# Kernel optimization log

Measured on AMD Instinct MI355X. Metric: run time of the kernel, lower is better.

The kernel has to match this reference:

```python
import jax, jax.numpy as jnp
import numpy as np

DIM = 768
HEADS = 12
E = 8
TOPK = 2
EPS = 1e-5


def layer_norm(x, g, b):
    m = jnp.mean(x, axis=-1, keepdims=True)
    v = jnp.mean((x - m) ** 2, axis=-1, keepdims=True)
    return (x - m) * jax.lax.rsqrt(v + EPS) * g + b


def setup_inputs() -> dict:
    key = jax.random.key(0)
    ks = jax.random.split(key, 12)
    B, N, C = 16, 1024, DIM
    s = 0.02
    return {
        "x": jax.random.normal(ks[0], (B, N, C), jnp.float32),
        "noise": jax.random.normal(ks[1], (B, N, E), jnp.float32),
        "ln1_g": jnp.ones((C,), jnp.float32),
        "ln1_b": jnp.zeros((C,), jnp.float32),
        "qkv_w": jax.random.normal(ks[2], (C, 3 * C), jnp.float32) * s,  # pre-transposed
        "proj_w": jax.random.normal(ks[3], (C, C), jnp.float32) * s,
        "proj_b": jnp.zeros((C,), jnp.float32),
        "ln2_g": jnp.ones((C,), jnp.float32),
        "ln2_b": jnp.zeros((C,), jnp.float32),
        "route_w": jax.random.normal(ks[4], (C, E), jnp.float32) * s,
        "route_b": jnp.zeros((E,), jnp.float32),
        "rln_g": jnp.ones((E,), jnp.float32),
        "rln_b": jnp.zeros((E,), jnp.float32),
        "expert_w": jax.random.normal(ks[5], (E, C, C), jnp.float32) * s,  # [E, in, out]
        "expert_b": jnp.zeros((E, C), jnp.float32),
    }


def reference(x, noise, ln1_g, ln1_b, qkv_w, proj_w, proj_b, ln2_g, ln2_b,
              route_w, route_b, rln_g, rln_b, expert_w, expert_b):
    B, N, C = x.shape
    H = HEADS
    Dh = C // H
    scale = Dh ** -0.5

    # --- Attention branch ---
    h = layer_norm(x, ln1_g, ln1_b)
    qkv = (h @ qkv_w).reshape(B, N, 3, H, Dh)
    q, k, v = qkv[:, :, 0], qkv[:, :, 1], qkv[:, :, 2]  # [B,N,H,Dh]
    attn = jnp.einsum('bnhd,bmhd->bhnm', q, k) * scale
    attn = jax.nn.softmax(attn, axis=-1)
    o = jnp.einsum('bhnm,bmhd->bnhd', attn, v).reshape(B, N, C)
    x = x + o @ proj_w + proj_b

    # --- MoE branch ---
    h = layer_norm(x, ln2_g, ln2_b)
    logits = layer_norm(h @ route_w + route_b, rln_g, rln_b)  # [B,N,E]
    rw = jax.nn.softmax(logits, axis=-1) + noise * (1.0 / E)
    topk_w, topk_idx = jax.lax.top_k(rw, TOPK)               # [B,N,K]
    topk_w = jax.nn.softmax(topk_w, axis=-1)

    # dense all-expert compute (faithful to source): [B,N,E,C]
    expert_out = jnp.einsum('bnc,ecd->bned', h, expert_w) + expert_b
    selected = jnp.take_along_axis(expert_out, topk_idx[..., None], axis=2)  # [B,N,K,C]
    moe = jnp.sum(selected * topk_w[..., None], axis=2)
    return x + moe
```

## Files before the change

kernel.cpp:

```cpp
#include <hip/hip_runtime.h>
#include <hip/hip_fp16.h>

typedef unsigned short u16;
typedef unsigned int u32;
typedef _Float16 f16;
typedef short bf16x8 __attribute__((ext_vector_type(8)));
typedef f16 f16x8 __attribute__((ext_vector_type(8)));
typedef float f32x4 __attribute__((ext_vector_type(4)));
typedef u32 u32x4 __attribute__((ext_vector_type(4)));

#define TOKENS 16384
#define CDIM 768
#define NEXP 8

#define QSCALE 0.18033688011112043f

__device__ __forceinline__ u16 f2b(float f) {
  u32 u = __float_as_uint(f);
  return (u16)((u + 0x7fffu + ((u >> 16) & 1u)) >> 16);
}
__device__ __forceinline__ u16 f16bits(f16 x) {
  union { f16 f; u16 u; } c;
  c.f = x;
  return c.u;
}
__device__ __forceinline__ f32x4 mfma_bf(bf16x8 a, bf16x8 b, f32x4 c) {
  return __builtin_amdgcn_mfma_f32_16x16x32_bf16(a, b, c, 0, 0, 0);
}
__device__ __forceinline__ f32x4 mfma_h(f16x8 a, f16x8 b, f32x4 c) {
  return __builtin_amdgcn_mfma_f32_16x16x32_f16(a, b, c, 0, 0, 0);
}
__device__ __forceinline__ void split8(const float* v, f16x8& h, f16x8& l) {
#pragma unroll
  for (int i = 0; i < 8; i++) {
    const f16 hh = (f16)v[i];
    h[i] = hh;
    l[i] = (f16)(v[i] - (float)hh);
  }
}

__global__ __launch_bounds__(256) void transpose_split_f16(
    const float* __restrict__ in, f16* __restrict__ oh, f16* __restrict__ ol,
    int K, int N) {
  __shared__ float tile[64][65];
  const int n0 = blockIdx.x * 64, k0 = blockIdx.y * 64;
#pragma unroll
  for (int i = 0; i < 16; i++) {
    const int s = threadIdx.x + i * 256;
    const int r = s >> 6, c = s & 63;
    tile[r][c] = in[(size_t)(k0 + r) * N + n0 + c];
  }
  __syncthreads();
#pragma unroll
  for (int i = 0; i < 16; i++) {
    const int s = threadIdx.x + i * 256;
    const int r = s >> 6, c = s & 63;
    const float v = tile[c][r];
    const f16 h = (f16)v;
    oh[(size_t)(n0 + r) * K + k0 + c] = h;
    ol[(size_t)(n0 + r) * K + k0 + c] = (f16)(v - (float)h);
  }
}

__global__ __launch_bounds__(256) void transpose_f32_bf16(
    const float* __restrict__ in, u16* __restrict__ out, int K, int N) {
  __shared__ u16 tile[64][65];
  const int z = blockIdx.z;
  in += (size_t)z * K * N;
  out += (size_t)z * K * N;
  const int n0 = blockIdx.x * 64, k0 = blockIdx.y * 64;
#pragma unroll
  for (int i = 0; i < 16; i++) {
    const int s = threadIdx.x + i * 256;
    const int r = s >> 6, c = s & 63;
    tile[r][c] = f2b(in[(size_t)(k0 + r) * N + n0 + c]);
  }
  __syncthreads();
#pragma unroll
  for (int i = 0; i < 16; i++) {
    const int s = threadIdx.x + i * 256;
    const int r = s >> 6, c = s & 63;
    out[(size_t)(n0 + r) * K + k0 + c] = tile[c][r];
  }
}

template <bool BF16OUT>
__global__ __launch_bounds__(256) void ln_rows(const float* __restrict__ in,
                                               const float* __restrict__ g,
                                               const float* __restrict__ bt,
                                               void* __restrict__ out) {
  const int row = blockIdx.x * 4 + (threadIdx.x >> 6);
  const int lane = threadIdx.x & 63;
  const size_t base = (size_t)row * CDIM;
  float v[12];
  float s = 0.f, ss = 0.f;
#pragma unroll
  for (int j = 0; j < 12; j++) {
    const int idx = lane + j * 64;
    v[j] = in[base + idx];
    s += v[j];
    ss += v[j] * v[j];
  }
#pragma unroll
  for (int m = 1; m < 64; m <<= 1) {
    s += __shfl_xor(s, m);
    ss += __shfl_xor(ss, m);
  }
  const float mean = s * (1.f / CDIM);
  const float var = ss * (1.f / CDIM) - mean * mean;
  const float rs = rsqrtf(var + 1e-5f);
#pragma unroll
  for (int j = 0; j < 12; j++) {
    const int idx = lane + j * 64;
    const float y = (v[j] - mean) * rs * g[idx] + bt[idx];
    if (BF16OUT)
      ((u16*)out)[base + idx] = f2b(y);
    else
      ((float*)out)[base + idx] = y;
  }
}

template <int EPI>
__global__ __launch_bounds__(256) void gemm_f16s(
    const float* __restrict__ A, const f16* __restrict__ Bth,
    const f16* __restrict__ Btl, float* __restrict__ C, int M, int N, int K,
    const float* __restrict__ bias, const float* __restrict__ xres,
    f16* __restrict__ Oh, f16* __restrict__ Ol, u32* __restrict__ Ov) {
  __shared__ f16 Ah[128 * 64];
  __shared__ f16 Al[128 * 64];
  __shared__ f16 Bh[128 * 64];
  __shared__ f16 Bl[128 * 64];
  const int tid = threadIdx.x;
  const int lane = tid & 63, wv = tid >> 6;
  const int wr = wv >> 1, wc = wv & 1;
  const int lm = lane & 15, lq = lane >> 4;
  const int m0 = blockIdx.y * 128, n0 = blockIdx.x * 128;
  f32x4 acc[4][4];
  const f32x4 z4 = {0.f, 0.f, 0.f, 0.f};
#pragma unroll
  for (int i = 0; i < 4; i++)
#pragma unroll
    for (int j = 0; j < 4; j++) acc[i][j] = z4;

  for (int k0 = 0; k0 < K; k0 += 64) {
    __syncthreads();
#pragma unroll
    for (int i = 0; i < 4; i++) {
      const int s = tid + i * 256;
      const int r = s >> 3, g = s & 7;
      float av[8];
      *(float4*)&av[0] = *(const float4*)(A + (size_t)(m0 + r) * K + k0 + g * 8);
      *(float4*)&av[4] =
          *(const float4*)(A + (size_t)(m0 + r) * K + k0 + g * 8 + 4);
      f16x8 hh, ll;
      split8(av, hh, ll);
      const int sw = r * 64 + ((g ^ (r & 7)) << 3);
      *(f16x8*)(&Ah[sw]) = hh;
      *(f16x8*)(&Al[sw]) = ll;
      *(f16x8*)(&Bh[sw]) = *(const f16x8*)(Bth + (size_t)(n0 + r) * K + k0 + g * 8);
      *(f16x8*)(&Bl[sw]) = *(const f16x8*)(Btl + (size_t)(n0 + r) * K + k0 + g * 8);
    }
    __syncthreads();
#pragma unroll
    for (int kx = 0; kx < 8; kx += 4) {
      f16x8 afh[4], afl[4], bfh[4], bfl[4];
#pragma unroll
      for (int i = 0; i < 4; i++) {
        const int ra = wr * 64 + i * 16 + lm;
        const int aw = ra * 64 + (((ra & 7) ^ (kx + lq)) << 3);
        afh[i] = *(const f16x8*)(&Ah[aw]);
        afl[i] = *(const f16x8*)(&Al[aw]);
        const int rb = wc * 64 + i * 16 + lm;
        const int bw = rb * 64 + (((rb & 7) ^ (kx + lq)) << 3);
        bfh[i] = *(const f16x8*)(&Bh[bw]);
        bfl[i] = *(const f16x8*)(&Bl[bw]);
      }
#pragma unroll
      for (int i = 0; i < 4; i++)
#pragma unroll
        for (int j = 0; j < 4; j++) {
          acc[i][j] = mfma_h(afh[i], bfh[j], acc[i][j]);
          acc[i][j] = mfma_h(afh[i], bfl[j], acc[i][j]);
          acc[i][j] = mfma_h(afl[i], bfh[j], acc[i][j]);
        }
    }
  }
#pragma unroll
  for (int i = 0; i < 4; i++)
#pragma unroll
    for (int r = 0; r < 4; r++) {
      const size_t row = m0 + wr * 64 + i * 16 + lq * 4 + r;
#pragma unroll
      for (int j = 0; j < 4; j++) {
        const int col = n0 + wc * 64 + j * 16 + lm;
        float v = acc[i][j][r];
        if constexpr (EPI == 0) {
          C[row * N + col] = v;
        } else if constexpr (EPI == 1) {
          v += bias[col] + xres[row * N + col];
          C[row * N + col] = v;
        } else {
          if (n0 < 768) v *= QSCALE;
          const f16 hh = (f16)v;
          const f16 ll = (f16)(v - (float)hh);
          if (n0 < 1536) {
            Oh[row * 1536 + col] = hh;
            Ol[row * 1536 + col] = ll;
          } else {
            Ov[row * 768 + (col - 1536)] =
                (u32)f16bits(hh) | ((u32)f16bits(ll) << 16);
          }
        }
      }
    }
}

__global__ __launch_bounds__(256) void attn_f16s(
    const f16* __restrict__ qkh, const f16* __restrict__ qkl,
    const u32* __restrict__ vI, float* __restrict__ o, int qb) {
  __shared__ f16 Kh[64 * 64];
  __shared__ f16 Kl[64 * 64];
  __shared__ f16 Vh[64 * 64];
  __shared__ f16 Vl[64 * 64];
  __shared__ f16 Ph[4 * 16 * 64];
  __shared__ f16 Pl[4 * 16 * 64];
  const int bz = blockIdx.z, h = blockIdx.y, qt = blockIdx.x;
  const int tid = threadIdx.x, wv = tid >> 6, lane = tid & 63;
  const int lm = lane & 15, lq = lane >> 4;

  f16x8 qh[2], ql[2];
  {
    const size_t qrow =
        (size_t)(bz * 1024 + qt * 64 + wv * 16 + lm) * 1536 + h * 64;
#pragma unroll
    for (int f = 0; f < 2; f++) {
      qh[f] = *(const f16x8*)(qkh + qrow + f * 32 + lq * 8);
      ql[f] = *(const f16x8*)(qkl + qrow + f * 32 + lq * 8);
    }
  }
  const f32x4 z4 = {0.f, 0.f, 0.f, 0.f};
  f32x4 oacc[4];
#pragma unroll
  for (int jb = 0; jb < 4; jb++) oacc[jb] = z4;
  float mrun[4], lrun[4];
#pragma unroll
  for (int r = 0; r < 4; r++) {
    mrun[r] = -1e30f;
    lrun[r] = 0.f;
  }
  const int vd = tid & 63;
  const int vkg = tid >> 6;
  f16* pwh = &Ph[wv * 16 * 64];
  f16* pwl = &Pl[wv * 16 * 64];

  for (int kt = 0; kt < 16; kt++) {
    __syncthreads();
#pragma unroll
    for (int i = 0; i < 2; i++) {
      const int s2 = tid + i * 256;
      const int r = s2 >> 3, g = s2 & 7;
      const size_t kb =
          (size_t)(bz * 1024 + kt * 64 + r) * 1536 + 768 + h * 64 + g * 8;
      const int sw = r * 64 + ((g ^ (r & 7)) << 3);
      *(f16x8*)(&Kh[sw]) = *(const f16x8*)(qkh + kb);
      *(f16x8*)(&Kl[sw]) = *(const f16x8*)(qkl + kb);
    }
#pragma unroll
    for (int sseg = 0; sseg < 2; sseg++) {
      const int k0v = vkg * 16 + sseg * 8;
      f16x8 hh, ll;
#pragma unroll
      for (int j = 0; j < 8; j++) {
        const u32 w = vI[(size_t)(bz * 1024 + kt * 64 + k0v + j) * 768 +
                         h * 64 + vd];
        ((u16*)&hh)[j] = (u16)(w & 0xffffu);
        ((u16*)&ll)[j] = (u16)(w >> 16);
      }
      const int g = k0v >> 3;
      const int sw = vd * 64 + ((g ^ (vd & 7)) << 3);
      *(f16x8*)(&Vh[sw]) = hh;
      *(f16x8*)(&Vl[sw]) = ll;
    }
    __syncthreads();

    f32x4 sa[4];
#pragma unroll
    for (int j = 0; j < 4; j++) sa[j] = z4;
#pragma unroll
    for (int kx = 0; kx < 8; kx += 4) {
      const f16x8 ah = qh[kx >> 2], al = ql[kx >> 2];
#pragma unroll
      for (int j = 0; j < 4; j++) {
        const int rb = j * 16 + lm;
        const int bw = rb * 64 + (((rb & 7) ^ (kx + lq)) << 3);
        const f16x8 bh = *(const f16x8*)(&Kh[bw]);
        const f16x8 bl = *(const f16x8*)(&Kl[bw]);
        sa[j] = mfma_h(ah, bh, sa[j]);
        sa[j] = mfma_h(ah, bl, sa[j]);
        sa[j] = mfma_h(al, bh, sa[j]);
      }
    }

#pragma unroll
    for (int r = 0; r < 4; r++) {
      float mx = fmaxf(fmaxf(sa[0][r], sa[1][r]), fmaxf(sa[2][r], sa[3][r]));
      mx = fmaxf(mx, __shfl_xor(mx, 1));
      mx = fmaxf(mx, __shfl_xor(mx, 2));
      mx = fmaxf(mx, __shfl_xor(mx, 4));
      mx = fmaxf(mx, __shfl_xor(mx, 8));
      const float mnew = fmaxf(mrun[r], mx);
      const float alpha = exp2f(mrun[r] - mnew);
      float ps = 0.f;
#pragma unroll
      for (int j = 0; j < 4; j++) {
        const float p = exp2f(sa[j][r] - mnew);
        sa[j][r] = p;
        ps += p;
      }
      ps += __shfl_xor(ps, 1);
      ps += __shfl_xor(ps, 2);
      ps += __shfl_xor(ps, 4);
      ps += __shfl_xor(ps, 8);
      lrun[r] = lrun[r] * alpha + ps;
      mrun[r] = mnew;
#pragma unroll
      for (int jb = 0; jb < 4; jb++) oacc[jb][r] *= alpha;
    }

#pragma unroll
    for (int j = 0; j < 4; j++)
#pragma unroll
      for (int r = 0; r < 4; r++) {
        const int qr = lq * 4 + r;
        const int key = j * 16 + lm;
        const int ad = qr * 64 + (((qr & 7) ^ (key >> 3)) << 3) + (key & 7);
        const float p = sa[j][r];
        const f16 ph = (f16)p;
        pwh[ad] = ph;
        pwl[ad] = (f16)(p - (float)ph);
      }
#pragma unroll
    for (int kx2 = 0; kx2 < 8; kx2 += 4) {
      const int pw = lm * 64 + (((lm & 7) ^ (kx2 + lq)) << 3);
      const f16x8 pah = *(const f16x8*)(&pwh[pw]);
      const f16x8 pal = *(const f16x8*)(&pwl[pw]);
#pragma unroll
      for (int jb = 0; jb < 4; jb++) {
        const int rb = jb * 16 + lm;
        const int vw = rb * 64 + (((rb & 7) ^ (kx2 + lq)) << 3);
        const f16x8 vh = *(const f16x8*)(&Vh[vw]);
        const f16x8 vl = *(const f16x8*)(&Vl[vw]);
        oacc[jb] = mfma_h(pah, vh, oacc[jb]);
        oacc[jb] = mfma_h(pah, vl, oacc[jb]);
        oacc[jb] = mfma_h(pal, vh, oacc[jb]);
      }
    }
  }
  const int gtok = (qb * 4 + bz) * 1024 + qt * 64;
#pragma unroll
  for (int r = 0; r < 4; r++) {
    const float inv = 1.f / lrun[r];
    const size_t row = (size_t)gtok + wv * 16 + lq * 4 + r;
#pragma unroll
    for (int jb = 0; jb < 4; jb++) {
      const int col = h * 64 + jb * 16 + lm;
      o[row * CDIM + col] = oacc[jb][r] * inv;
    }
  }
}

__global__ __launch_bounds__(256) void gemm_expert(
    const u16* __restrict__ A, const u16* __restrict__ Bt,
    __half* __restrict__ Cp, int N, int K, const float* __restrict__ bias,
    const int* __restrict__ counts, const int* __restrict__ eBase,
    const int* __restrict__ tokList, const float* __restrict__ wgtList) {
  __shared__ u16 As[128 * 64];
  __shared__ u16 Bs[128 * 64];
  const int did = blockIdx.x;
  const int e = did & 7;
  const int s = did >> 3;
  const int bx = s % 6;
  const int by = s / 6;
  const int cnt = counts[e];
  const int m0 = by * 128, n0 = bx * 128;
  if (m0 >= cnt) return;
  const int tid = threadIdx.x;
  const int lane = tid & 63, wv = tid >> 6;
  const int wr = wv >> 1, wc = wv & 1;
  const int lm = lane & 15, lq = lane >> 4;
  const u16* Bte = Bt + (size_t)e * N * K;
  const int* tokl = tokList + e * TOKENS;
  const float* wl = wgtList + e * TOKENS;
  const float* biasE = bias + e * N;
  const int base0 = eBase[e];

  const int r0 = tid >> 3, g = tid & 7;
  const int swz = (g ^ (r0 & 7)) << 3;
  const u16* ap[4];
  const u16* bp[4];
#pragma unroll
  for (int i = 0; i < 4; i++) {
    const int row = m0 + r0 + i * 32;
    const int tok = (row < cnt) ? tokl[row] : 0;
    ap[i] = A + (size_t)tok * K + g * 8;
    bp[i] = Bte + (size_t)(n0 + r0 + i * 32) * K + g * 8;
  }

  f32x4 acc[4][4];
  const f32x4 z4 = {0.f, 0.f, 0.f, 0.f};
#pragma unroll
  for (int i = 0; i < 4; i++)
#pragma unroll
    for (int j = 0; j < 4; j++) acc[i][j] = z4;

  u32x4 pa[4], pb[4];
#pragma unroll
  for (int i = 0; i < 4; i++) {
    pa[i] = *(const u32x4*)(ap[i]);
    pb[i] = *(const u32x4*)(bp[i]);
  }
#pragma unroll
  for (int i = 0; i < 4; i++) {
    *(u32x4*)(&As[(r0 + i * 32) * 64 + swz]) = pa[i];
    *(u32x4*)(&Bs[(r0 + i * 32) * 64 + swz]) = pb[i];
  }

  for (int k0 = 0; k0 < K; k0 += 64) {
    __syncthreads();
    const bool more = (k0 + 64) < K;
    if (more) {
#pragma unroll
      for (int i = 0; i < 4; i++) {
        pa[i] = *(const u32x4*)(ap[i] + k0 + 64);
        pb[i] = *(const u32x4*)(bp[i] + k0 + 64);
      }
    }
#pragma unroll
    for (int kx = 0; kx < 8; kx += 4) {
      bf16x8 af[4], bfv[4];
#pragma unroll
      for (int i = 0; i < 4; i++) {
        const int ra = wr * 64 + i * 16 + lm;
        af[i] = *(const bf16x8*)(&As[ra * 64 + (((ra & 7) ^ (kx + lq)) << 3)]);
        const int rb = wc * 64 + i * 16 + lm;
        bfv[i] = *(const bf16x8*)(&Bs[rb * 64 + (((rb & 7) ^ (kx + lq)) << 3)]);
      }
#pragma unroll
      for (int i = 0; i < 4; i++)
#pragma unroll
        for (int j = 0; j < 4; j++)
          acc[i][j] = mfma_bf(af[i], bfv[j], acc[i][j]);
    }
    __syncthreads();
    if (more) {
#pragma unroll
      for (int i = 0; i < 4; i++) {
        *(u32x4*)(&As[(r0 + i * 32) * 64 + swz]) = pa[i];
        *(u32x4*)(&Bs[(r0 + i * 32) * 64 + swz]) = pb[i];
      }
    }
  }
#pragma unroll
  for (int i = 0; i < 4; i++)
#pragma unroll
    for (int r = 0; r < 4; r++) {
      const int rowi = m0 + wr * 64 + i * 16 + lq * 4 + r;
      const bool live = (rowi < cnt);
      const float w = live ? wl[rowi] : 0.f;
      const size_t prow = live ? (size_t)(base0 + rowi) * (size_t)N : 0;
#pragma unroll
      for (int j = 0; j < 4; j++) {
        const int col = n0 + wc * 64 + j * 16 + lm;
        const float v = (acc[i][j][r] + biasE[col]) * w;
        const float vn = __shfl_xor(v, 1);
        if (live && (lm & 1) == 0) {
          *(__half2*)(Cp + prow + col) =
              __halves2half2(__float2half(v), __float2half(vn));
        }
      }
    }
}

__global__ __launch_bounds__(256) void router_kernel(
    const float* __restrict__ x2, const float* __restrict__ g2,
    const float* __restrict__ b2, const float* __restrict__ rw,
    const float* __restrict__ rb, const float* __restrict__ rlng,
    const float* __restrict__ rlnb, const float* __restrict__ noise,
    int* __restrict__ eidx, float* __restrict__ ewgt) {
  const int token = blockIdx.x * 4 + (threadIdx.x >> 6);
  const int lane = threadIdx.x & 63;
  const size_t base = (size_t)token * CDIM;
  float v[12];
  float s = 0.f, ss = 0.f;
#pragma unroll
  for (int j = 0; j < 12; j++) {
    const int idx = lane + j * 64;
    v[j] = x2[base + idx];
    s += v[j];
    ss += v[j] * v[j];
  }
#pragma unroll
  for (int m = 1; m < 64; m <<= 1) {
    s += __shfl_xor(s, m);
    ss += __shfl_xor(ss, m);
  }
  const float mean = s * (1.f / CDIM);
  const float var = ss * (1.f / CDIM) - mean * mean;
  const float rs = rsqrtf(var + 1e-5f);

  float acc[8];
#pragma unroll
  for (int e = 0; e < 8; e++) acc[e] = 0.f;
#pragma unroll
  for (int j = 0; j < 12; j++) {
    const int d = lane + j * 64;
    const float hv = (v[j] - mean) * rs * g2[d] + b2[d];
    const f32x4 w0v = *(const f32x4*)(rw + (size_t)d * 8);
    const f32x4 w1v = *(const f32x4*)(rw + (size_t)d * 8 + 4);
#pragma unroll
    for (int e = 0; e < 4; e++) {
      acc[e] += hv * w0v[e];
      acc[e + 4] += hv * w1v[e];
    }
  }
#pragma unroll
  for (int m = 1; m < 64; m <<= 1)
#pragma unroll
    for (int e = 0; e < 8; e++) acc[e] += __shfl_xor(acc[e], m);

  float y[8];
  float emean = 0.f;
#pragma unroll
  for (int e = 0; e < 8; e++) {
    y[e] = acc[e] + rb[e];
    emean += y[e];
  }
  emean *= 0.125f;
  float evar = 0.f;
#pragma unroll
  for (int e = 0; e < 8; e++) {
    const float d = y[e] - emean;
    evar += d * d;
  }
  evar *= 0.125f;
  const float ers = rsqrtf(evar + 1e-5f);
  float lg[8];
  float mx = -1e30f;
#pragma unroll
  for (int e = 0; e < 8; e++) {
    lg[e] = (y[e] - emean) * ers * rlng[e] + rlnb[e];
    mx = fmaxf(mx, lg[e]);
  }
  float se = 0.f;
#pragma unroll
  for (int e = 0; e < 8; e++) {
    lg[e] = expf(lg[e] - mx);
    se += lg[e];
  }
  const float inv = 1.f / se;
  float r2[8];
#pragma unroll
  for (int e = 0; e < 8; e++)
    r2[e] = lg[e] * inv + noise[(size_t)token * 8 + e] * 0.125f;

  int e0 = 0;
  float v0 = r2[0];
#pragma unroll
  for (int e = 1; e < 8; e++)
    if (r2[e] > v0) {
      v0 = r2[e];
      e0 = e;
    }
  int e1 = -1;
  float v1 = -1e30f;
#pragma unroll
  for (int e = 0; e < 8; e++)
    if (e != e0 && r2[e] > v1) {
      v1 = r2[e];
      e1 = e;
    }
  const float w0 = 1.f / (1.f + expf(v1 - v0));
  if (lane == 0) {
    eidx[token * 2] = e0;
    eidx[token * 2 + 1] = e1;
    ewgt[token * 2] = w0;
    ewgt[token * 2 + 1] = 1.f - w0;
  }
}

__global__ __launch_bounds__(256) void build_lists(
    const int* __restrict__ eidx, const float* __restrict__ ewgt,
    int* __restrict__ counts, int* __restrict__ tokL, float* __restrict__ wgtL,
    int* __restrict__ posL) {
  const int e = blockIdx.x;
  __shared__ int cnt;
  if (threadIdx.x == 0) cnt = 0;
  __syncthreads();
  const int lane = threadIdx.x & 63;
  for (int t = threadIdx.x; t < TOKENS; t += 256) {
#pragma unroll
    for (int k = 0; k < 2; k++) {
      const bool match = (eidx[t * 2 + k] == e);
      const unsigned long long mb = __ballot(match);
      if (mb) {
        const int leader = __ffsll((unsigned long long)mb) - 1;
        int base = 0;
        if (lane == leader) base = atomicAdd(&cnt, __popcll(mb));
        base = __shfl(base, leader);
        if (match) {
          const int rank = __popcll(mb & ((1ull << lane) - 1ull));
          tokL[e * TOKENS + base + rank] = t;
          wgtL[e * TOKENS + base + rank] = ewgt[t * 2 + k];
          posL[t * 2 + k] = base + rank;
        }
      }
    }
  }
  __syncthreads();
  if (threadIdx.x == 0) counts[e] = cnt;
}

__global__ void prefix_counts(const int* __restrict__ counts,
                              int* __restrict__ eBase) {
  if (threadIdx.x == 0) {
    int s = 0;
#pragma unroll
    for (int e = 0; e < NEXP; e++) {
      eBase[e] = s;
      s += counts[e];
    }
    eBase[NEXP] = s;
  }
}

__global__ __launch_bounds__(256) void combine_moe(
    float* __restrict__ x2, const __half* __restrict__ Cp,
    const int* __restrict__ eidx, const int* __restrict__ posL,
    const int* __restrict__ eBase) {
  const int t = blockIdx.x * 4 + (threadIdx.x >> 6);
  const int lane = threadIdx.x & 63;
  const int e0 = eidx[t * 2], e1 = eidx[t * 2 + 1];
  const size_t q0 = (size_t)(eBase[e0] + posL[t * 2]) * CDIM;
  const size_t q1 = (size_t)(eBase[e1] + posL[t * 2 + 1]) * CDIM;
  const size_t base = (size_t)t * CDIM;
#pragma unroll
  for (int j = 0; j < 12; j++) {
    const int d = lane + j * 64;
    const float m =
        __half2float(Cp[q0 + d]) + __half2float(Cp[q1 + d]);
    x2[base + d] += m;
  }
}

__global__ __launch_bounds__(256) void copy_f32(const float* __restrict__ in,
                                                float* __restrict__ out) {
  const int i = (blockIdx.x * 256 + threadIdx.x) * 4;
  *(float4*)(out + i) = *(const float4*)(in + i);
}

extern "C" void kernel_launch(void* const* d_in, const int* in_sizes, int n_in,
                              void* d_out, int out_size, void* d_ws,
                              size_t ws_size, hipStream_t stream) {
  const float* x = (const float*)d_in[0];
  const float* noise = (const float*)d_in[1];
  const float* ln1_g = (const float*)d_in[2];
  const float* ln1_b = (const float*)d_in[3];
  const float* qkv_w = (const float*)d_in[4];
  const float* proj_w = (const float*)d_in[5];
  const float* proj_b = (const float*)d_in[6];
  const float* ln2_g = (const float*)d_in[7];
  const float* ln2_b = (const float*)d_in[8];
  const float* route_w = (const float*)d_in[9];
  const float* route_b = (const float*)d_in[10];
  const float* rln_g = (const float*)d_in[11];
  const float* rln_b = (const float*)d_in[12];
  const float* expert_w = (const float*)d_in[13];
  const float* expert_b = (const float*)d_in[14];

  char* ws = (char*)d_ws;
  float* x2f = (float*)(ws);
  f16* qkh = (f16*)(ws + 50331648);
  f16* qkl = (f16*)(ws + 62914560);
  u32* vIq = (u32*)(ws + 75497472);
  u16* exp_wt = (u16*)(ws + 50331648);
  u16* h2 = (u16*)(ws + 59768832);
  int* counts = (int*)(ws + 84934656);
  int* eBase = (int*)(ws + 84934784);
  int* eidx = (int*)(ws + 84934912);
  float* ewgt = (float*)(ws + 85065984);
  int* tokL = (int*)(ws + 85197056);
  float* wgtL = (float*)(ws + 85721344);
  int* posL = (int*)(ws + 86245632);
  f16* qkvw_h = (f16*)(ws + 88080384);
  f16* qkvw_l = (f16*)(ws + 91619328);
  f16* projw_h = (f16*)(ws + 95158272);
  f16* projw_l = (f16*)(ws + 96337920);
  float* h1f = (float*)d_out;
  __half* cperm = (__half*)d_out;

  const dim3 blk(256);
  transpose_split_f16<<<dim3(36, 12), blk, 0, stream>>>(qkv_w, qkvw_h, qkvw_l,
                                                        768, 2304);
  transpose_split_f16<<<dim3(12, 12), blk, 0, stream>>>(proj_w, projw_h,
                                                        projw_l, 768, 768);
  ln_rows<false><<<dim3(4096), blk, 0, stream>>>(x, ln1_g, ln1_b, h1f);
  for (int q = 0; q < 4; q++) {
    gemm_f16s<2><<<dim3(18, 32), blk, 0, stream>>>(
        h1f + (size_t)q * 4096 * 768, qkvw_h, qkvw_l, nullptr, 4096, 2304,
        768, nullptr, nullptr, qkh, qkl, vIq);
    attn_f16s<<<dim3(16, 12, 4), blk, 0, stream>>>(qkh, qkl, vIq, h1f, q);
  }
  gemm_f16s<1><<<dim3(6, 128), blk, 0, stream>>>(h1f, projw_h, projw_l, x2f,
                                                 16384, 768, 768, proj_b, x,
                                                 nullptr, nullptr, nullptr);
  ln_rows<true><<<dim3(4096), blk, 0, stream>>>(x2f, ln2_g, ln2_b, h2);
  transpose_f32_bf16<<<dim3(12, 12, 8), blk, 0, stream>>>(expert_w, exp_wt,
                                                          768, 768);
  router_kernel<<<dim3(4096), blk, 0, stream>>>(x2f, ln2_g, ln2_b, route_w,
                                                route_b, rln_g, rln_b, noise,
                                                eidx, ewgt);
  build_lists<<<dim3(8), blk, 0, stream>>>(eidx, ewgt, counts, tokL, wgtL,
                                           posL);
  prefix_counts<<<dim3(1), dim3(64), 0, stream>>>(counts, eBase);
  gemm_expert<<<dim3(6144), blk, 0, stream>>>(h2, exp_wt, cperm, 768, 768,
                                              expert_b, counts, eBase, tokL,
                                              wgtL);
  combine_moe<<<dim3(4096), blk, 0, stream>>>(x2f, cperm, eidx, posL, eBase);
  copy_f32<<<dim3(12288), blk, 0, stream>>>(x2f, (float*)d_out);
}
```

Baseline: 1.088 ms.

## Split attention over key halves with merge kernel; fuse LN2 into router

The attention kernel now splits the 16 key tiles into two halves, doubling grid size. Each half writes unnormalized partial outputs plus running max and sum to workspace, and a new merge kernel combines them with log-sum-exp rescaling. The P staging buffers now reuse K shared memory, which needs an extra barrier but cuts LDS use. Separately, the LN2 normalisation that wrote h2 is folded into the router kernel, removing one full pass over x2. The split adds extra global traffic for the partial outputs and an extra launch per chunk.

```diff
diff --git a/kernel.cpp b/kernel.cpp
--- a/kernel.cpp
+++ b/kernel.cpp
@@ -217,14 +217,15 @@
 
 __global__ __launch_bounds__(256) void attn_f16s(
     const f16* __restrict__ qkh, const f16* __restrict__ qkl,
-    const u32* __restrict__ vI, float* __restrict__ o, int qb) {
+    const u32* __restrict__ vI, float* __restrict__ opart,
+    float* __restrict__ ml) {
   __shared__ f16 Kh[64 * 64];
   __shared__ f16 Kl[64 * 64];
   __shared__ f16 Vh[64 * 64];
   __shared__ f16 Vl[64 * 64];
-  __shared__ f16 Ph[4 * 16 * 64];
-  __shared__ f16 Pl[4 * 16 * 64];
-  const int bz = blockIdx.z, h = blockIdx.y, qt = blockIdx.x;
+  const int z = blockIdx.z;
+  const int bz = z & 3, sp = z >> 2;
+  const int h = blockIdx.y, qt = blockIdx.x;
   const int tid = threadIdx.x, wv = tid >> 6, lane = tid & 63;
   const int lm = lane & 15, lq = lane >> 4;
 
@@ -250,10 +251,10 @@
   }
   const int vd = tid & 63;
   const int vkg = tid >> 6;
-  f16* pwh = &Ph[wv * 16 * 64];
-  f16* pwl = &Pl[wv * 16 * 64];
-
-  for (int kt = 0; kt < 16; kt++) {
+  f16* pwh = &Kh[wv * 16 * 64];
+  f16* pwl = &Kl[wv * 16 * 64];
+
+  for (int kt = sp * 8; kt < sp * 8 + 8; kt++) {
     __syncthreads();
 #pragma unroll
     for (int i = 0; i < 2; i++) {
@@ -327,6 +328,8 @@
       for (int jb = 0; jb < 4; jb++) oacc[jb][r] *= alpha;
     }
 
+    __syncthreads();
+
 #pragma unroll
     for (int j = 0; j < 4; j++)
 #pragma unroll
@@ -356,16 +359,42 @@
       }
     }
   }
-  const int gtok = (qb * 4 + bz) * 1024 + qt * 64;
 #pragma unroll
   for (int r = 0; r < 4; r++) {
-    const float inv = 1.f / lrun[r];
-    const size_t row = (size_t)gtok + wv * 16 + lq * 4 + r;
+    const int row = bz * 1024 + qt * 64 + wv * 16 + lq * 4 + r;
+    const size_t obase = ((size_t)sp * 4096 + row) * CDIM;
 #pragma unroll
     for (int jb = 0; jb < 4; jb++) {
       const int col = h * 64 + jb * 16 + lm;
-      o[row * CDIM + col] = oacc[jb][r] * inv;
-    }
+      opart[obase + col] = oacc[jb][r];
+    }
+    if (lm == 0) {
+      const size_t mb = (((size_t)sp * 4096 + row) * 12 + h) * 2;
+      ml[mb] = mrun[r];
+      ml[mb + 1] = lrun[r];
+    }
+  }
+}
+
+__global__ __launch_bounds__(256) void attn_merge(
+    const float* __restrict__ opart, const float* __restrict__ ml,
+    float* __restrict__ o, int qb) {
+  const int row = blockIdx.x * 4 + (threadIdx.x >> 6);
+  const int lane = threadIdx.x & 63;
+  const size_t r0 = (size_t)row * CDIM;
+  const size_t r1 = (size_t)(4096 + row) * CDIM;
+  const size_t orow = ((size_t)qb * 4096 + row) * CDIM;
+#pragma unroll
+  for (int j = 0; j < 12; j++) {
+    const int d = lane + j * 64;
+    const size_t mb0 = ((size_t)row * 12 + j) * 2;
+    const size_t mb1 = ((size_t)(4096 + row) * 12 + j) * 2;
+    const float m0 = ml[mb0], l0 = ml[mb0 + 1];
+    const float m1 = ml[mb1], l1 = ml[mb1 + 1];
+    const float m = fmaxf(m0, m1);
+    const float w0 = exp2f(m0 - m), w1 = exp2f(m1 - m);
+    const float inv = 1.f / (l0 * w0 + l1 * w1);
+    o[orow + d] = (opart[r0 + d] * w0 + opart[r1 + d] * w1) * inv;
   }
 }
 
@@ -481,12 +510,12 @@
     }
 }
 
-__global__ __launch_bounds__(256) void router_kernel(
+__global__ __launch_bounds__(256) void ln2_router(
     const float* __restrict__ x2, const float* __restrict__ g2,
     const float* __restrict__ b2, const float* __restrict__ rw,
     const float* __restrict__ rb, const float* __restrict__ rlng,
     const float* __restrict__ rlnb, const float* __restrict__ noise,
-    int* __restrict__ eidx, float* __restrict__ ewgt) {
+    u16* __restrict__ h2, int* __restrict__ eidx, float* __restrict__ ewgt) {
   const int token = blockIdx.x * 4 + (threadIdx.x >> 6);
   const int lane = threadIdx.x & 63;
   const size_t base = (size_t)token * CDIM;
@@ -515,6 +544,7 @@
   for (int j = 0; j < 12; j++) {
     const int d = lane + j * 64;
     const float hv = (v[j] - mean) * rs * g2[d] + b2[d];
+    h2[base + d] = f2b(hv);
     const f32x4 w0v = *(const f32x4*)(rw + (size_t)d * 8);
     const f32x4 w1v = *(const f32x4*)(rw + (size_t)d * 8 + 4);
 #pragma unroll
@@ -679,6 +709,8 @@
 
   char* ws = (char*)d_ws;
   float* x2f = (float*)(ws);
+  float* opart = (float*)(ws);
+  float* mlbuf = (float*)(ws + 25165824);
   f16* qkh = (f16*)(ws + 50331648);
   f16* qkl = (f16*)(ws + 62914560);
   u32* vIq = (u32*)(ws + 75497472);
@@ -708,17 +740,18 @@
     gemm_f16s<2><<<dim3(18, 32), blk, 0, stream>>>(
         h1f + (size_t)q * 4096 * 768, qkvw_h, qkvw_l, nullptr, 4096, 2304,
         768, nullptr, nullptr, qkh, qkl, vIq);
-    attn_f16s<<<dim3(16, 12, 4), blk, 0, stream>>>(qkh, qkl, vIq, h1f, q);
+    attn_f16s<<<dim3(16, 12, 8), blk, 0, stream>>>(qkh, qkl, vIq, opart,
+                                                   mlbuf);
+    attn_merge<<<dim3(1024), blk, 0, stream>>>(opart, mlbuf, h1f, q);
   }
   gemm_f16s<1><<<dim3(6, 128), blk, 0, stream>>>(h1f, projw_h, projw_l, x2f,
                                                  16384, 768, 768, proj_b, x,
                                                  nullptr, nullptr, nullptr);
-  ln_rows<true><<<dim3(4096), blk, 0, stream>>>(x2f, ln2_g, ln2_b, h2);
+  ln2_router<<<dim3(4096), blk, 0, stream>>>(x2f, ln2_g, ln2_b, route_w,
+                                             route_b, rln_g, rln_b, noise, h2,
+                                             eidx, ewgt);
   transpose_f32_bf16<<<dim3(12, 12, 8), blk, 0, stream>>>(expert_w, exp_wt,
                                                           768, 768);
-  router_kernel<<<dim3(4096), blk, 0, stream>>>(x2f, ln2_g, ln2_b, route_w,
-                                                route_b, rln_g, rln_b, noise,
-                                                eidx, ewgt);
   build_lists<<<dim3(8), blk, 0, stream>>>(eidx, ewgt, counts, tokL, wgtL,
                                            posL);
   prefix_counts<<<dim3(1), dim3(64), 0, stream>>>(counts, eBase);
```

New measurement: 1.132 ms. +4.0%, slower.
